# Kernel tuning notes

Hardware: AMD Instinct MI355X
Metric: run time of the kernel (lower is better)

## Reference

```python
import jax, jax.numpy as jnp
import numpy as np

# Module constants (from init_kwargs)
IN_PLANES = 32
NUM_FILTERS = 4
MAX_H = 128
MAX_W = 128
REPARAM_FACTOR = 8
REPARAM_H = MAX_H * REPARAM_FACTOR  # 1024
REPARAM_W = MAX_W * REPARAM_FACTOR  # 1024
NORMALIZE = True
BATCH = 8


def _init_box_params(key):
    """Random valid boxes (mimics reset_parameters), returned in the
    reparametrized (scaled-down) form stored in the module."""
    k1, k2, k3, k4 = jax.random.split(key, 4)
    shape = (IN_PLANES, NUM_FILTERS)
    # actual box coordinates: x_min < 0 < x_max, comfortably inside the image
    x_min = jax.random.uniform(k1, shape, minval=-MAX_H / 3.0, maxval=-2.0)
    x_max = jax.random.uniform(k2, shape, minval=2.0, maxval=MAX_H / 3.0)
    y_min = jax.random.uniform(k3, shape, minval=-MAX_W / 3.0, maxval=-2.0)
    y_max = jax.random.uniform(k4, shape, minval=2.0, maxval=MAX_W / 3.0)
    # store in reparametrized form (divide by reparametrization scale)
    return (x_min / REPARAM_H, x_max / REPARAM_H,
            y_min / REPARAM_W, y_max / REPARAM_W)


def setup_inputs() -> dict:
    key = jax.random.key(0)
    k_in, k_box = jax.random.split(key)
    inp = jax.random.normal(k_in, (BATCH, IN_PLANES, MAX_H, MAX_W), dtype=jnp.float32)
    x_min, x_max, y_min, y_max = _init_box_params(k_box)
    return {"input": inp,
            "x_min": x_min.astype(jnp.float32), "x_max": x_max.astype(jnp.float32),
            "y_min": y_min.astype(jnp.float32), "y_max": y_max.astype(jnp.float32)}


def reference(input, x_min, x_max, y_min, y_max):
    B, C, H, W = input.shape
    F = x_min.shape[1]

    # undo reparametrization -> actual continuous box coordinates
    xmin = x_min * REPARAM_H
    xmax = x_max * REPARAM_H
    ymin = y_min * REPARAM_W
    ymax = y_max * REPARAM_W

    # integral image with a zero row/col on top/left: ii[b,c,i,j] = sum input[:i,:j]
    ii = jnp.pad(jnp.cumsum(jnp.cumsum(input, axis=2), axis=3),
                 ((0, 0), (0, 0), (1, 0), (1, 0)))  # [B,C,H+1,W+1]

    h_idx = jnp.arange(H, dtype=input.dtype)
    w_idx = jnp.arange(W, dtype=input.dtype)

    # continuous corner coordinates per (channel, filter, output position),
    # clipped into the valid integral-image domain (zero padding outside)
    xs_t = jnp.clip(h_idx[None, None, :] + xmin[:, :, None], 0.0, H)        # [C,F,H]
    xs_b = jnp.clip(h_idx[None, None, :] + xmax[:, :, None] + 1.0, 0.0, H)  # [C,F,H]
    ys_l = jnp.clip(w_idx[None, None, :] + ymin[:, :, None], 0.0, W)        # [C,F,W]
    ys_r = jnp.clip(w_idx[None, None, :] + ymax[:, :, None] + 1.0, 0.0, W)  # [C,F,W]

    c_idx = jnp.arange(C)[:, None, None]  # [C,1,1]

    def x_interp(xs):
        # linear interpolation of integral-image rows at continuous x coords
        x0f = jnp.clip(jnp.floor(xs), 0.0, H - 1.0)   # [C,F,H]
        fx = xs - x0f
        x0 = x0f.astype(jnp.int32)
        r0 = ii[:, c_idx, x0, :]       # [B,C,F,H,W+1]
        r1 = ii[:, c_idx, x0 + 1, :]   # [B,C,F,H,W+1]
        return (1.0 - fx)[None, :, :, :, None] * r0 + fx[None, :, :, :, None] * r1

    def y_interp(rows, ys):
        # linear interpolation along W of x-interpolated integral rows
        y0f = jnp.clip(jnp.floor(ys), 0.0, W - 1.0)   # [C,F,W]
        fy = ys - y0f
        y0 = y0f.astype(jnp.int32)[None, :, :, None, :]  # [1,C,F,1,W]
        tgt = rows.shape[:-1] + (W,)
        g0 = jnp.take_along_axis(rows, jnp.broadcast_to(y0, tgt), axis=-1)
        g1 = jnp.take_along_axis(rows, jnp.broadcast_to(y0 + 1, tgt), axis=-1)
        return (1.0 - fy)[None, :, :, None, :] * g0 + fy[None, :, :, None, :] * g1

    rows_t = x_interp(xs_t)  # top edge
    rows_b = x_interp(xs_b)  # bottom edge

    # inclusion-exclusion over the four bilinearly-sampled corners
    out = (y_interp(rows_b, ys_r) - y_interp(rows_b, ys_l)) \
        - (y_interp(rows_t, ys_r) - y_interp(rows_t, ys_l))   # [B,C,F,H,W]

    if NORMALIZE:
        area = (xmax - xmin + 1.0) * (ymax - ymin + 1.0)  # [C,F]
        out = out / area[None, :, :, None, None]

    return out.reshape(B, C * F, H, W)
```

## Files before the change

kernel.cpp:

```cpp
#include <hip/hip_runtime.h>

#define BATCH 8
#define CC 32
#define FF 4
#define HH 128
#define WW 128
#define STRIDE 130
#define RP 1024.0f
#define NTHREADS 1024
#define NWAVES 16
#define CH 8
#define DEW 240
#define DEBASE 48

__global__ __launch_bounds__(NTHREADS) void boxconv_kernel(
    const float* __restrict__ in,
    const float* __restrict__ xmin_p,
    const float* __restrict__ xmax_p,
    const float* __restrict__ ymin_p,
    const float* __restrict__ ymax_p,
    float* __restrict__ out)
{
    __shared__ float ii[(HH + 1) * STRIDE];
    __shared__ float de[NWAVES * DEW];
    __shared__ float partial[8 * 128];

    const int plane = blockIdx.x;
    const int c = plane & (CC - 1);
    const int tid = threadIdx.x;
    const int wave = tid >> 6;
    const int lane = tid & 63;
    const float* inp = in + (size_t)plane * (HH * WW);

    for (int i4 = tid; i4 < (HH * WW) / 4; i4 += NTHREADS) {
        const float4 v = ((const float4*)inp)[i4];
        const int idx = i4 << 2;
        const int x = idx >> 7;
        const int y = idx & (WW - 1);
        float* dst = &ii[(x + 1) * STRIDE + (y + 1)];
        dst[0] = v.x; dst[1] = v.y; dst[2] = v.z; dst[3] = v.w;
    }
    if (tid <= HH) {
        ii[tid] = 0.0f;
        ii[tid * STRIDE] = 0.0f;
    }
    if (lane < DEBASE) de[wave * DEW + lane] = 0.0f;
    __syncthreads();

    {
        const int row = tid & 127, seg = tid >> 7;
        float* p = &ii[(row + 1) * STRIDE + 1 + seg * 16];
        float v[16];
        float s = 0.0f;
        #pragma unroll
        for (int j = 0; j < 16; ++j) { s += p[j]; v[j] = s; }
        partial[seg * 128 + row] = s;
        __syncthreads();
        float off = 0.0f;
        for (int k = 0; k < seg; ++k) off += partial[k * 128 + row];
        #pragma unroll
        for (int j = 0; j < 16; ++j) p[j] = v[j] + off;
    }
    __syncthreads();

    {
        const int col = tid & 127, seg = tid >> 7;
        float* p = &ii[(seg * 16 + 1) * STRIDE + col + 1];
        float v[16];
        float s = 0.0f;
        #pragma unroll
        for (int j = 0; j < 16; ++j) { s += p[j * STRIDE]; v[j] = s; }
        partial[seg * 128 + col] = s;
        __syncthreads();
        float off = 0.0f;
        for (int k = 0; k < seg; ++k) off += partial[k * 128 + col];
        #pragma unroll
        for (int j = 0; j < 16; ++j) p[j * STRIDE] = v[j] + off;
    }
    __syncthreads();

    float* De = &de[wave * DEW];
    const int h0 = wave * CH;

    for (int f = 0; f < FF; ++f) {
        const int pidx = c * FF + f;
        const float xmn = xmin_p[pidx] * RP;
        const float xmx = xmax_p[pidx] * RP;
        const float ymn = ymin_p[pidx] * RP;
        const float ymx = ymax_p[pidx] * RP;
        const float inv_area = 1.0f / ((xmx - xmn + 1.0f) * (ymx - ymn + 1.0f));
        const float ktf = floorf(xmn);          const int kt = (int)ktf;  const float ft = xmn - ktf;
        const float kbf = floorf(xmx + 1.0f);   const int kb = (int)kbf;  const float fb = xmx + 1.0f - kbf;
        const float klf = floorf(ymn);          const int kl = (int)klf;  const float fl = ymn - klf;
        const float krf = floorf(ymx + 1.0f);   const int kr = (int)krf;  const float fr = ymx + 1.0f - krf;
        const float gt = 1.0f - ft, gb = 1.0f - fb, gl = 1.0f - fl, gr = 1.0f - fr;
        const int al = kl & ~1, dl = kl - al;
        const int ar = kr & ~1, dr = kr - ar;
        const float* Lp = &De[DEBASE + al + 2 * lane];
        const float* Rp = &De[DEBASE + ar + 2 * lane];
        float* outf = out + ((size_t)plane * FF + f) * (HH * WW);

        const int xt = h0 + kt;
        const int xb = h0 + kb;
        const float* p0 = &ii[min(max(xt, 0), 128) * STRIDE];
        const float* q0 = &ii[min(max(xb, 0), 128) * STRIDE];
        float2 tp = *(const float2*)&p0[2 * lane];
        float  tp2 = p0[128];
        float2 bp = *(const float2*)&q0[2 * lane];
        float  bp2 = q0[128];

        #pragma unroll
        for (int j = 0; j < CH; ++j) {
            const float* p = &ii[min(max(xt + j + 1, 0), 128) * STRIDE];
            const float* q = &ii[min(max(xb + j + 1, 0), 128) * STRIDE];
            const float2 tc = *(const float2*)&p[2 * lane];
            const float  tc2 = p[128];
            const float2 bc = *(const float2*)&q[2 * lane];
            const float  bc2 = q[128];

            const float d0   = (gb * bp.x + fb * bc.x) - (gt * tp.x + ft * tc.x);
            const float d1   = (gb * bp.y + fb * bc.y) - (gt * tp.y + ft * tc.y);
            const float d128 = (gb * bp2  + fb * bc2 ) - (gt * tp2  + ft * tc2 );

            *(float2*)&De[DEBASE + 2 * lane] = make_float2(d0, d1);
            De[DEBASE + 128 + lane] = d128;

            const float2 vL0 = *(const float2*)(Lp);
            const float2 vL1 = *(const float2*)(Lp + 2);
            const float2 vR0 = *(const float2*)(Rp);
            const float2 vR1 = *(const float2*)(Rp + 2);
            const float La = dl ? vL0.y : vL0.x;
            const float Lb = dl ? vL1.x : vL0.y;
            const float Lc = dl ? vL1.y : vL1.x;
            const float Ra = dr ? vR0.y : vR0.x;
            const float Rb = dr ? vR1.x : vR0.y;
            const float Rc = dr ? vR1.y : vR1.x;

            const float o0 = (gr * Ra + fr * Rb - gl * La - fl * Lb) * inv_area;
            const float o1 = (gr * Rb + fr * Rc - gl * Lb - fl * Lc) * inv_area;
            *(float2*)&outf[(h0 + j) * WW + 2 * lane] = make_float2(o0, o1);

            tp = tc; tp2 = tc2; bp = bc; bp2 = bc2;
        }
    }
}

extern "C" void kernel_launch(void* const* d_in, const int* in_sizes, int n_in,
                              void* d_out, int out_size, void* d_ws, size_t ws_size,
                              hipStream_t stream) {
    const float* inp    = (const float*)d_in[0];
    const float* x_min  = (const float*)d_in[1];
    const float* x_max  = (const float*)d_in[2];
    const float* y_min  = (const float*)d_in[3];
    const float* y_max  = (const float*)d_in[4];
    float* out = (float*)d_out;

    dim3 grid(BATCH * CC);
    dim3 block(NTHREADS);
    boxconv_kernel<<<grid, block, 0, stream>>>(inp, x_min, x_max, y_min, y_max, out);
}
```

Before: 96.69 us.

## Split into integral-image kernel and parallel box-filter kernel via workspace

Splits the fused kernel in two. The first kernel builds each plane's integral image in shared memory and writes it to a global workspace. The second launches 2048 small blocks, one per plane, filter and half-height, which read integral rows from global memory (likely L2-resident) and produce the output. This raises the number of blocks beyond 256 to fill the GPU better, at the cost of a workspace round trip, a second launch, and global instead of LDS loads for the integral rows.

```diff
diff --git a/kernel.cpp b/kernel.cpp
--- a/kernel.cpp
+++ b/kernel.cpp
@@ -7,32 +7,21 @@
 #define WW 128
 #define STRIDE 130
 #define RP 1024.0f
-#define NTHREADS 1024
-#define NWAVES 16
-#define CH 8
+#define PS 16896
 #define DEW 240
 #define DEBASE 48
 
-__global__ __launch_bounds__(NTHREADS) void boxconv_kernel(
-    const float* __restrict__ in,
-    const float* __restrict__ xmin_p,
-    const float* __restrict__ xmax_p,
-    const float* __restrict__ ymin_p,
-    const float* __restrict__ ymax_p,
-    float* __restrict__ out)
+__global__ __launch_bounds__(1024) void ii_kernel(const float* __restrict__ in,
+                                                  float* __restrict__ ws)
 {
-    __shared__ float ii[(HH + 1) * STRIDE];
-    __shared__ float de[NWAVES * DEW];
+    __shared__ float ii[(HH + 1) * STRIDE + 4];
     __shared__ float partial[8 * 128];
 
     const int plane = blockIdx.x;
-    const int c = plane & (CC - 1);
     const int tid = threadIdx.x;
-    const int wave = tid >> 6;
-    const int lane = tid & 63;
     const float* inp = in + (size_t)plane * (HH * WW);
 
-    for (int i4 = tid; i4 < (HH * WW) / 4; i4 += NTHREADS) {
+    for (int i4 = tid; i4 < (HH * WW) / 4; i4 += 1024) {
         const float4 v = ((const float4*)inp)[i4];
         const int idx = i4 << 2;
         const int x = idx >> 7;
@@ -40,18 +29,13 @@
         float* dst = &ii[(x + 1) * STRIDE + (y + 1)];
         dst[0] = v.x; dst[1] = v.y; dst[2] = v.z; dst[3] = v.w;
     }
-    if (tid <= HH) {
-        ii[tid] = 0.0f;
-        ii[tid * STRIDE] = 0.0f;
-    }
-    if (lane < DEBASE) de[wave * DEW + lane] = 0.0f;
+    if (tid <= HH) { ii[tid] = 0.0f; ii[tid * STRIDE] = 0.0f; }
     __syncthreads();
 
     {
         const int row = tid & 127, seg = tid >> 7;
         float* p = &ii[(row + 1) * STRIDE + 1 + seg * 16];
-        float v[16];
-        float s = 0.0f;
+        float v[16]; float s = 0.0f;
         #pragma unroll
         for (int j = 0; j < 16; ++j) { s += p[j]; v[j] = s; }
         partial[seg * 128 + row] = s;
@@ -62,12 +46,10 @@
         for (int j = 0; j < 16; ++j) p[j] = v[j] + off;
     }
     __syncthreads();
-
     {
         const int col = tid & 127, seg = tid >> 7;
         float* p = &ii[(seg * 16 + 1) * STRIDE + col + 1];
-        float v[16];
-        float s = 0.0f;
+        float v[16]; float s = 0.0f;
         #pragma unroll
         for (int j = 0; j < 16; ++j) { s += p[j * STRIDE]; v[j] = s; }
         partial[seg * 128 + col] = s;
@@ -79,69 +61,90 @@
     }
     __syncthreads();
 
+    float4* dst = (float4*)(ws + (size_t)plane * PS);
+    for (int i = tid; i < 4193; i += 1024)
+        dst[i] = *(const float4*)&ii[4 * i];
+}
+
+__global__ __launch_bounds__(256) void box_kernel(
+    const float* __restrict__ ws,
+    const float* __restrict__ xmin_p,
+    const float* __restrict__ xmax_p,
+    const float* __restrict__ ymin_p,
+    const float* __restrict__ ymax_p,
+    float* __restrict__ out)
+{
+    __shared__ float de[4 * DEW];
+
+    const int bid = blockIdx.x;
+    const int plane = bid & 255;
+    const int rest = bid >> 8;
+    const int f = rest & 3;
+    const int hh = rest >> 2;
+    const int c = plane & (CC - 1);
+    const int tid = threadIdx.x;
+    const int wave = tid >> 6;
+    const int lane = tid & 63;
+    const float* iip = ws + (size_t)plane * PS;
+
     float* De = &de[wave * DEW];
-    const int h0 = wave * CH;
+    if (lane < DEBASE) De[lane] = 0.0f;
 
-    for (int f = 0; f < FF; ++f) {
-        const int pidx = c * FF + f;
-        const float xmn = xmin_p[pidx] * RP;
-        const float xmx = xmax_p[pidx] * RP;
-        const float ymn = ymin_p[pidx] * RP;
-        const float ymx = ymax_p[pidx] * RP;
-        const float inv_area = 1.0f / ((xmx - xmn + 1.0f) * (ymx - ymn + 1.0f));
-        const float ktf = floorf(xmn);          const int kt = (int)ktf;  const float ft = xmn - ktf;
-        const float kbf = floorf(xmx + 1.0f);   const int kb = (int)kbf;  const float fb = xmx + 1.0f - kbf;
-        const float klf = floorf(ymn);          const int kl = (int)klf;  const float fl = ymn - klf;
-        const float krf = floorf(ymx + 1.0f);   const int kr = (int)krf;  const float fr = ymx + 1.0f - krf;
-        const float gt = 1.0f - ft, gb = 1.0f - fb, gl = 1.0f - fl, gr = 1.0f - fr;
-        const int al = kl & ~1, dl = kl - al;
-        const int ar = kr & ~1, dr = kr - ar;
-        const float* Lp = &De[DEBASE + al + 2 * lane];
-        const float* Rp = &De[DEBASE + ar + 2 * lane];
-        float* outf = out + ((size_t)plane * FF + f) * (HH * WW);
+    const int pidx = c * FF + f;
+    const float xmn = xmin_p[pidx] * RP;
+    const float xmx = xmax_p[pidx] * RP;
+    const float ymn = ymin_p[pidx] * RP;
+    const float ymx = ymax_p[pidx] * RP;
+    const float inv_area = 1.0f / ((xmx - xmn + 1.0f) * (ymx - ymn + 1.0f));
+    const float ktf = floorf(xmn);          const int kt = (int)ktf;  const float ft = xmn - ktf;
+    const float kbf = floorf(xmx + 1.0f);   const int kb = (int)kbf;  const float fb = xmx + 1.0f - kbf;
+    const float klf = floorf(ymn);          const int kl = (int)klf;  const float fl = ymn - klf;
+    const float krf = floorf(ymx + 1.0f);   const int kr = (int)krf;  const float fr = ymx + 1.0f - krf;
+    const float gt = 1.0f - ft, gb = 1.0f - fb, gl = 1.0f - fl, gr = 1.0f - fr;
+    const int al = kl & ~1, dl = kl - al;
+    const int ar = kr & ~1, dr = kr - ar;
+    const float* Lp = &De[DEBASE + al + 2 * lane];
+    const float* Rp = &De[DEBASE + ar + 2 * lane];
+    float* outf = out + ((size_t)plane * FF + f) * (HH * WW);
 
-        const int xt = h0 + kt;
-        const int xb = h0 + kb;
-        const float* p0 = &ii[min(max(xt, 0), 128) * STRIDE];
-        const float* q0 = &ii[min(max(xb, 0), 128) * STRIDE];
-        float2 tp = *(const float2*)&p0[2 * lane];
-        float  tp2 = p0[128];
-        float2 bp = *(const float2*)&q0[2 * lane];
-        float  bp2 = q0[128];
+    const int h0 = hh * 64 + wave * 16;
+    const int xt = h0 + kt;
+    const int xb = h0 + kb;
+    const float* p0 = &iip[min(max(xt, 0), 128) * STRIDE];
+    const float* q0 = &iip[min(max(xb, 0), 128) * STRIDE];
+    float2 tp = *(const float2*)&p0[2 * lane];  float tp2 = p0[128];
+    float2 bp = *(const float2*)&q0[2 * lane];  float bp2 = q0[128];
 
-        #pragma unroll
-        for (int j = 0; j < CH; ++j) {
-            const float* p = &ii[min(max(xt + j + 1, 0), 128) * STRIDE];
-            const float* q = &ii[min(max(xb + j + 1, 0), 128) * STRIDE];
-            const float2 tc = *(const float2*)&p[2 * lane];
-            const float  tc2 = p[128];
-            const float2 bc = *(const float2*)&q[2 * lane];
-            const float  bc2 = q[128];
+    #pragma unroll 4
+    for (int j = 0; j < 16; ++j) {
+        const float* p = &iip[min(max(xt + j + 1, 0), 128) * STRIDE];
+        const float* q = &iip[min(max(xb + j + 1, 0), 128) * STRIDE];
+        const float2 tc = *(const float2*)&p[2 * lane];  const float tc2 = p[128];
+        const float2 bc = *(const float2*)&q[2 * lane];  const float bc2 = q[128];
 
-            const float d0   = (gb * bp.x + fb * bc.x) - (gt * tp.x + ft * tc.x);
-            const float d1   = (gb * bp.y + fb * bc.y) - (gt * tp.y + ft * tc.y);
-            const float d128 = (gb * bp2  + fb * bc2 ) - (gt * tp2  + ft * tc2 );
+        const float d0   = (gb * bp.x + fb * bc.x) - (gt * tp.x + ft * tc.x);
+        const float d1   = (gb * bp.y + fb * bc.y) - (gt * tp.y + ft * tc.y);
+        const float d128 = (gb * bp2  + fb * bc2 ) - (gt * tp2  + ft * tc2 );
 
-            *(float2*)&De[DEBASE + 2 * lane] = make_float2(d0, d1);
-            De[DEBASE + 128 + lane] = d128;
+        *(float2*)&De[DEBASE + 2 * lane] = make_float2(d0, d1);
+        De[DEBASE + 128 + lane] = d128;
 
-            const float2 vL0 = *(const float2*)(Lp);
-            const float2 vL1 = *(const float2*)(Lp + 2);
-            const float2 vR0 = *(const float2*)(Rp);
-            const float2 vR1 = *(const float2*)(Rp + 2);
-            const float La = dl ? vL0.y : vL0.x;
-            const float Lb = dl ? vL1.x : vL0.y;
-            const float Lc = dl ? vL1.y : vL1.x;
-            const float Ra = dr ? vR0.y : vR0.x;
-            const float Rb = dr ? vR1.x : vR0.y;
-            const float Rc = dr ? vR1.y : vR1.x;
+        const float2 vL0 = *(const float2*)(Lp);
+        const float2 vL1 = *(const float2*)(Lp + 2);
+        const float2 vR0 = *(const float2*)(Rp);
+        const float2 vR1 = *(const float2*)(Rp + 2);
+        const float La = dl ? vL0.y : vL0.x;
+        const float Lb = dl ? vL1.x : vL0.y;
+        const float Lc = dl ? vL1.y : vL1.x;
+        const float Ra = dr ? vR0.y : vR0.x;
+        const float Rb = dr ? vR1.x : vR0.y;
+        const float Rc = dr ? vR1.y : vR1.x;
 
-            const float o0 = (gr * Ra + fr * Rb - gl * La - fl * Lb) * inv_area;
-            const float o1 = (gr * Rb + fr * Rc - gl * Lb - fl * Lc) * inv_area;
-            *(float2*)&outf[(h0 + j) * WW + 2 * lane] = make_float2(o0, o1);
+        const float o0 = (gr * Ra + fr * Rb - gl * La - fl * Lb) * inv_area;
+        const float o1 = (gr * Rb + fr * Rc - gl * Lb - fl * Lc) * inv_area;
+        *(float2*)&outf[(h0 + j) * WW + 2 * lane] = make_float2(o0, o1);
 
-            tp = tc; tp2 = tc2; bp = bc; bp2 = bc2;
-        }
+        tp = tc; tp2 = tc2; bp = bc; bp2 = bc2;
     }
 }
 
@@ -154,8 +157,8 @@
     const float* y_min  = (const float*)d_in[3];
     const float* y_max  = (const float*)d_in[4];
     float* out = (float*)d_out;
+    float* ws  = (float*)d_ws;
 
-    dim3 grid(BATCH * CC);
-    dim3 block(NTHREADS);
-    boxconv_kernel<<<grid, block, 0, stream>>>(inp, x_min, x_max, y_min, y_max, out);
+    ii_kernel<<<dim3(BATCH * CC), dim3(1024), 0, stream>>>(inp, ws);
+    box_kernel<<<dim3(8 * BATCH * CC), dim3(256), 0, stream>>>(ws, x_min, x_max, y_min, y_max, out);
 }
```

Result: slower. 103.1 us (+6.7%).

## Fuse row prefix scan into global load and interleave two filters per pass

Applied to the files above, without the earlier changes.

The row-wise prefix sum is now computed directly in registers from global float4 loads, with a wave shuffle scan across 8-lane segments. This removes the separate LDS staging pass, one barrier and the partial-sum reads. The output loop now handles two filters at a time, each with its own per-wave scratch buffer, so independent LDS and global store work from both filters can interleave and hide latency. In exchange it doubles the scratch LDS and raises register pressure.

```diff
diff --git a/kernel.cpp b/kernel.cpp
--- a/kernel.cpp
+++ b/kernel.cpp
@@ -22,7 +22,7 @@
     float* __restrict__ out)
 {
     __shared__ float ii[(HH + 1) * STRIDE];
-    __shared__ float de[NWAVES * DEW];
+    __shared__ float de[NWAVES * 2 * DEW];
     __shared__ float partial[8 * 128];
 
     const int plane = blockIdx.x;
@@ -32,45 +32,41 @@
     const int lane = tid & 63;
     const float* inp = in + (size_t)plane * (HH * WW);
 
-    for (int i4 = tid; i4 < (HH * WW) / 4; i4 += NTHREADS) {
-        const float4 v = ((const float4*)inp)[i4];
-        const int idx = i4 << 2;
-        const int x = idx >> 7;
-        const int y = idx & (WW - 1);
-        float* dst = &ii[(x + 1) * STRIDE + (y + 1)];
-        dst[0] = v.x; dst[1] = v.y; dst[2] = v.z; dst[3] = v.w;
-    }
-    if (tid <= HH) {
-        ii[tid] = 0.0f;
-        ii[tid * STRIDE] = 0.0f;
-    }
-    if (lane < DEBASE) de[wave * DEW + lane] = 0.0f;
-    __syncthreads();
+    float* De0 = &de[(wave * 2 + 0) * DEW];
+    float* De1 = &de[(wave * 2 + 1) * DEW];
 
     {
-        const int row = tid & 127, seg = tid >> 7;
-        float* p = &ii[(row + 1) * STRIDE + 1 + seg * 16];
+        const int r = tid >> 3, s = tid & 7;
+        const float4* src = (const float4*)(inp + r * WW + s * 16);
+        const float4 A = src[0], B = src[1], C4 = src[2], D4 = src[3];
+        float t[16] = {A.x,A.y,A.z,A.w, B.x,B.y,B.z,B.w,
+                       C4.x,C4.y,C4.z,C4.w, D4.x,D4.y,D4.z,D4.w};
         float v[16];
-        float s = 0.0f;
+        float ssum = 0.0f;
         #pragma unroll
-        for (int j = 0; j < 16; ++j) { s += p[j]; v[j] = s; }
-        partial[seg * 128 + row] = s;
-        __syncthreads();
-        float off = 0.0f;
-        for (int k = 0; k < seg; ++k) off += partial[k * 128 + row];
+        for (int k = 0; k < 16; ++k) { ssum += t[k]; v[k] = ssum; }
+        float run = ssum;
         #pragma unroll
-        for (int j = 0; j < 16; ++j) p[j] = v[j] + off;
+        for (int d = 1; d < 8; d <<= 1) {
+            const float o = __shfl_up(run, (unsigned)d, 8);
+            if ((lane & 7) >= d) run += o;
+        }
+        const float off = run - ssum;
+        float* dst = &ii[(r + 1) * STRIDE + 1 + s * 16];
+        #pragma unroll
+        for (int k = 0; k < 16; ++k) dst[k] = v[k] + off;
     }
+    if (tid <= HH) { ii[tid] = 0.0f; ii[tid * STRIDE] = 0.0f; }
+    if (lane < DEBASE) { De0[lane] = 0.0f; De1[lane] = 0.0f; }
     __syncthreads();
 
     {
         const int col = tid & 127, seg = tid >> 7;
         float* p = &ii[(seg * 16 + 1) * STRIDE + col + 1];
-        float v[16];
-        float s = 0.0f;
+        float v[16]; float sum = 0.0f;
         #pragma unroll
-        for (int j = 0; j < 16; ++j) { s += p[j * STRIDE]; v[j] = s; }
-        partial[seg * 128 + col] = s;
+        for (int j = 0; j < 16; ++j) { sum += p[j * STRIDE]; v[j] = sum; }
+        partial[seg * 128 + col] = sum;
         __syncthreads();
         float off = 0.0f;
         for (int k = 0; k < seg; ++k) off += partial[k * 128 + col];
@@ -79,68 +75,78 @@
     }
     __syncthreads();
 
-    float* De = &de[wave * DEW];
     const int h0 = wave * CH;
+    for (int fp = 0; fp < 2; ++fp) {
+        int   kt[2], kb[2], dl[2], dr[2], xt[2], xb[2];
+        float ft_[2], fb_[2], gt_[2], gb_[2], fl_[2], fr_[2], gl_[2], gr_[2], ia_[2];
+        const float* Lp[2]; const float* Rp[2];
+        float* Deb[2] = {De0, De1};
+        float* outf[2];
+        #pragma unroll
+        for (int u = 0; u < 2; ++u) {
+            const int f = fp * 2 + u;
+            const int pidx = c * FF + f;
+            const float xmn = xmin_p[pidx] * RP;
+            const float xmx = xmax_p[pidx] * RP;
+            const float ymn = ymin_p[pidx] * RP;
+            const float ymx = ymax_p[pidx] * RP;
+            ia_[u] = 1.0f / ((xmx - xmn + 1.0f) * (ymx - ymn + 1.0f));
+            const float ktf = floorf(xmn);        kt[u] = (int)ktf;  ft_[u] = xmn - ktf;
+            const float kbf = floorf(xmx + 1.0f); kb[u] = (int)kbf;  fb_[u] = xmx + 1.0f - kbf;
+            const float klf = floorf(ymn);        const int kl = (int)klf;  fl_[u] = ymn - klf;
+            const float krf = floorf(ymx + 1.0f); const int kr = (int)krf;  fr_[u] = ymx + 1.0f - krf;
+            gt_[u] = 1.0f - ft_[u]; gb_[u] = 1.0f - fb_[u];
+            gl_[u] = 1.0f - fl_[u]; gr_[u] = 1.0f - fr_[u];
+            const int al = kl & ~1; dl[u] = kl - al;
+            const int ar = kr & ~1; dr[u] = kr - ar;
+            Lp[u] = &Deb[u][DEBASE + al + 2 * lane];
+            Rp[u] = &Deb[u][DEBASE + ar + 2 * lane];
+            outf[u] = out + ((size_t)plane * FF + f) * (HH * WW);
+            xt[u] = h0 + kt[u];
+            xb[u] = h0 + kb[u];
+        }
+        float2 tp[2], bp[2]; float tp2[2], bp2[2];
+        #pragma unroll
+        for (int u = 0; u < 2; ++u) {
+            const float* p0 = &ii[min(max(xt[u], 0), 128) * STRIDE];
+            const float* q0 = &ii[min(max(xb[u], 0), 128) * STRIDE];
+            tp[u] = *(const float2*)&p0[2 * lane];  tp2[u] = p0[128];
+            bp[u] = *(const float2*)&q0[2 * lane];  bp2[u] = q0[128];
+        }
 
-    for (int f = 0; f < FF; ++f) {
-        const int pidx = c * FF + f;
-        const float xmn = xmin_p[pidx] * RP;
-        const float xmx = xmax_p[pidx] * RP;
-        const float ymn = ymin_p[pidx] * RP;
-        const float ymx = ymax_p[pidx] * RP;
-        const float inv_area = 1.0f / ((xmx - xmn + 1.0f) * (ymx - ymn + 1.0f));
-        const float ktf = floorf(xmn);          const int kt = (int)ktf;  const float ft = xmn - ktf;
-        const float kbf = floorf(xmx + 1.0f);   const int kb = (int)kbf;  const float fb = xmx + 1.0f - kbf;
-        const float klf = floorf(ymn);          const int kl = (int)klf;  const float fl = ymn - klf;
-        const float krf = floorf(ymx + 1.0f);   const int kr = (int)krf;  const float fr = ymx + 1.0f - krf;
-        const float gt = 1.0f - ft, gb = 1.0f - fb, gl = 1.0f - fl, gr = 1.0f - fr;
-        const int al = kl & ~1, dl = kl - al;
-        const int ar = kr & ~1, dr = kr - ar;
-        const float* Lp = &De[DEBASE + al + 2 * lane];
-        const float* Rp = &De[DEBASE + ar + 2 * lane];
-        float* outf = out + ((size_t)plane * FF + f) * (HH * WW);
+        #pragma unroll 4
+        for (int j = 0; j < CH; ++j) {
+            #pragma unroll
+            for (int u = 0; u < 2; ++u) {
+                const float* p = &ii[min(max(xt[u] + j + 1, 0), 128) * STRIDE];
+                const float* q = &ii[min(max(xb[u] + j + 1, 0), 128) * STRIDE];
+                const float2 tc = *(const float2*)&p[2 * lane];  const float tc2 = p[128];
+                const float2 bc = *(const float2*)&q[2 * lane];  const float bc2 = q[128];
 
-        const int xt = h0 + kt;
-        const int xb = h0 + kb;
-        const float* p0 = &ii[min(max(xt, 0), 128) * STRIDE];
-        const float* q0 = &ii[min(max(xb, 0), 128) * STRIDE];
-        float2 tp = *(const float2*)&p0[2 * lane];
-        float  tp2 = p0[128];
-        float2 bp = *(const float2*)&q0[2 * lane];
-        float  bp2 = q0[128];
+                const float d0   = (gb_[u] * bp[u].x + fb_[u] * bc.x) - (gt_[u] * tp[u].x + ft_[u] * tc.x);
+                const float d1   = (gb_[u] * bp[u].y + fb_[u] * bc.y) - (gt_[u] * tp[u].y + ft_[u] * tc.y);
+                const float d128 = (gb_[u] * bp2[u]  + fb_[u] * bc2 ) - (gt_[u] * tp2[u]  + ft_[u] * tc2 );
 
-        #pragma unroll
-        for (int j = 0; j < CH; ++j) {
-            const float* p = &ii[min(max(xt + j + 1, 0), 128) * STRIDE];
-            const float* q = &ii[min(max(xb + j + 1, 0), 128) * STRIDE];
-            const float2 tc = *(const float2*)&p[2 * lane];
-            const float  tc2 = p[128];
-            const float2 bc = *(const float2*)&q[2 * lane];
-            const float  bc2 = q[128];
+                *(float2*)&Deb[u][DEBASE + 2 * lane] = make_float2(d0, d1);
+                Deb[u][DEBASE + 128 + lane] = d128;
 
-            const float d0   = (gb * bp.x + fb * bc.x) - (gt * tp.x + ft * tc.x);
-            const float d1   = (gb * bp.y + fb * bc.y) - (gt * tp.y + ft * tc.y);
-            const float d128 = (gb * bp2  + fb * bc2 ) - (gt * tp2  + ft * tc2 );
+                const float2 vL0 = *(const float2*)(Lp[u]);
+                const float2 vL1 = *(const float2*)(Lp[u] + 2);
+                const float2 vR0 = *(const float2*)(Rp[u]);
+                const float2 vR1 = *(const float2*)(Rp[u] + 2);
+                const float La = dl[u] ? vL0.y : vL0.x;
+                const float Lb = dl[u] ? vL1.x : vL0.y;
+                const float Lc = dl[u] ? vL1.y : vL1.x;
+                const float Ra = dr[u] ? vR0.y : vR0.x;
+                const float Rb = dr[u] ? vR1.x : vR0.y;
+                const float Rc = dr[u] ? vR1.y : vR1.x;
 
-            *(float2*)&De[DEBASE + 2 * lane] = make_float2(d0, d1);
-            De[DEBASE + 128 + lane] = d128;
+                const float o0 = (gr_[u] * Ra + fr_[u] * Rb - gl_[u] * La - fl_[u] * Lb) * ia_[u];
+                const float o1 = (gr_[u] * Rb + fr_[u] * Rc - gl_[u] * Lb - fl_[u] * Lc) * ia_[u];
+                *(float2*)&outf[u][(h0 + j) * WW + 2 * lane] = make_float2(o0, o1);
 
-            const float2 vL0 = *(const float2*)(Lp);
-            const float2 vL1 = *(const float2*)(Lp + 2);
-            const float2 vR0 = *(const float2*)(Rp);
-            const float2 vR1 = *(const float2*)(Rp + 2);
-            const float La = dl ? vL0.y : vL0.x;
-            const float Lb = dl ? vL1.x : vL0.y;
-            const float Lc = dl ? vL1.y : vL1.x;
-            const float Ra = dr ? vR0.y : vR0.x;
-            const float Rb = dr ? vR1.x : vR0.y;
-            const float Rc = dr ? vR1.y : vR1.x;
-
-            const float o0 = (gr * Ra + fr * Rb - gl * La - fl * Lb) * inv_area;
-            const float o1 = (gr * Rb + fr * Rc - gl * Lb - fl * Lc) * inv_area;
-            *(float2*)&outf[(h0 + j) * WW + 2 * lane] = make_float2(o0, o1);
-
-            tp = tc; tp2 = tc2; bp = bc; bp2 = bc2;
+                tp[u] = tc; tp2[u] = tc2; bp[u] = bc; bp2[u] = bc2;
+            }
         }
     }
 }
```

Result: slower. 99.71 us (+3.1%).
